# Kernel optimization log

Measured on AMD Instinct MI355X. Metric: run time of the kernel, lower is better.

## Reference

```python
import jax, jax.numpy as jnp
import numpy as np

B, S, E, H = 4, 2048, 1024, 16
D = E // H  # d_k = 64
NEG = -1000000000.0  # matches torch masked_fill constant


def setup_inputs() -> dict:
    rk = jax.random.key(0)
    kq, kk, kv, km = jax.random.split(rk, 4)
    query = jax.random.normal(kq, (B, S, E), dtype=jnp.float32)
    key = jax.random.normal(kk, (B, S, E), dtype=jnp.float32)
    value = jax.random.normal(kv, (B, S, E), dtype=jnp.float32)
    mask = jax.random.randint(km, (B, S, S), 0, 2, dtype=jnp.int32)
    return {"query": query, "key": key, "value": value, "mask": mask}


def _split_heads(x):
    # (B, S, E) -> (B, H, S, D)
    return x.reshape(B, S, H, D).transpose(0, 2, 1, 3)


def reference(query, key, value, mask):
    q = _split_heads(query)
    k = _split_heads(key)
    v = _split_heads(value)
    scale = np.float32(1.0 / np.sqrt(D))
    scores = jnp.einsum('bhqd,bhkd->bhqk', q, k) * scale  # (B,H,S,S)
    scores = jnp.where(mask[:, None, :, :] == 0, jnp.float32(NEG), scores)
    weights = jax.nn.softmax(scores, axis=-1)
    attn = jnp.einsum('bhqk,bhkd->bhqd', weights, v)  # (B,H,S,D)
    concat = attn.transpose(0, 2, 1, 3).reshape(B, S, E)
    return concat
```

## Files before the change

### kernel.cpp

```cpp
#include <hip/hip_runtime.h>
#include <hip/hip_bf16.h>
#include <math.h>

constexpr int B = 4, S = 2048, E = 1024, H = 16, D = 64;
constexpr float NEGF = -1000000000.0f;
constexpr float KSCALE = 0.125f * 1.44269504f;

typedef __attribute__((ext_vector_type(8))) short short8;
typedef __attribute__((ext_vector_type(16))) float f32x16;

__device__ inline unsigned pk2(float a, float b) {
    unsigned ua = __builtin_bit_cast(unsigned, a) + 0x8000u;
    unsigned ub = __builtin_bit_cast(unsigned, b) + 0x8000u;
    return __builtin_amdgcn_perm(ub, ua, 0x07060302u);
}
__device__ inline void gl_lds16(const void* g, void* l) {
    __builtin_amdgcn_global_load_lds(
        (const __attribute__((address_space(1))) unsigned int*)g,
        (__attribute__((address_space(3))) unsigned int*)l, 16, 0, 0);
}
__device__ inline void plswap(unsigned& a, unsigned& b) {
    asm volatile("v_permlane32_swap_b32 %0, %1" : "+v"(a), "+v"(b));
}

constexpr size_t WS_K  = 0;
constexpr size_t WS_VT = 18874368;
constexpr size_t WS_MB = 37748736;
constexpr size_t WS_NEED = 54525952;

__global__ void prep_all(const float* __restrict__ K, const float* __restrict__ V,
                         const int* __restrict__ M, char* __restrict__ ws) {
    __shared__ float Vf[64][69];
    const int bid = blockIdx.x, tid = threadIdx.x;

    {
        int g = bid * 256 + tid;
        int rowd = g >> 2, qtr = g & 3;
        int b = rowd >> 15, h = (rowd >> 11) & 15, s = rowd & 2047;
        const float* p = K + ((size_t)(b * S + s)) * E + h * 64 + qtr * 16;
        float4 v0 = *(const float4*)(p + 0),  v1 = *(const float4*)(p + 4);
        float4 v2 = *(const float4*)(p + 8),  v3 = *(const float4*)(p + 12);
        uint4 o0, o1;
        o0.x = pk2(v0.x * KSCALE, v0.y * KSCALE); o0.y = pk2(v0.z * KSCALE, v0.w * KSCALE);
        o0.z = pk2(v1.x * KSCALE, v1.y * KSCALE); o0.w = pk2(v1.z * KSCALE, v1.w * KSCALE);
        o1.x = pk2(v2.x * KSCALE, v2.y * KSCALE); o1.y = pk2(v2.z * KSCALE, v2.w * KSCALE);
        o1.z = pk2(v3.x * KSCALE, v3.y * KSCALE); o1.w = pk2(v3.z * KSCALE, v3.w * KSCALE);
        char* d = ws + WS_K + (size_t)rowd * 144 + qtr * 32;
        *(uint4*)d = o0; *(uint4*)(d + 16) = o1;
        if (qtr == 3) {
            uint4 z; z.x = z.y = z.z = z.w = 0;
            *(uint4*)(d + 32) = z;
        }
    }

    {
        int bh = bid >> 5, kt = bid & 31;
        int b = bh >> 4, h = bh & 15;
        {
            int r = tid >> 2, c4 = (tid & 3) * 16;
            const float* p = V + ((size_t)(b * S + kt * 64 + r)) * E + h * 64 + c4;
            float4 a = *(const float4*)(p + 0), bb = *(const float4*)(p + 4);
            float4 c = *(const float4*)(p + 8), dd = *(const float4*)(p + 12);
            *(float4*)&Vf[r][c4 + 0] = a;  *(float4*)&Vf[r][c4 + 4] = bb;
            *(float4*)&Vf[r][c4 + 8] = c;  *(float4*)&Vf[r][c4 + 12] = dd;
        }
        __syncthreads();
        int d = tid >> 2, sq = (tid & 3) * 16;
        float v[16];
#pragma unroll
        for (int i = 0; i < 16; ++i) v[i] = Vf[sq + i][d];
        uint4 o0, o1;
        o0.x = pk2(v[0], v[1]);   o0.y = pk2(v[2], v[3]);
        o0.z = pk2(v[4], v[5]);   o0.w = pk2(v[6], v[7]);
        o1.x = pk2(v[8], v[9]);   o1.y = pk2(v[10], v[11]);
        o1.z = pk2(v[12], v[13]); o1.w = pk2(v[14], v[15]);
        char* o = ws + WS_VT + ((size_t)(bh * 32 + kt)) * 9216 + d * 144 + sq * 2;
        *(uint4*)o = o0; *(uint4*)(o + 16) = o1;
        if (sq == 48) {
            uint4 z; z.x = z.y = z.z = z.w = 0;
            *(uint4*)(o + 32) = z;
        }
    }

    {
        unsigned* Mb = (unsigned*)(ws + WS_MB);
        const int t = bid * 256 + tid;
#pragma unroll
        for (int it = 0; it < 8; ++it) {
            int gidx = it * 524288 + t;
            int4 mv = *((const int4*)M + gidx);
            unsigned d = (mv.x ? 0xFFu : 0u) | (mv.y ? 0xFF00u : 0u)
                       | (mv.z ? 0xFF0000u : 0u) | (mv.w ? 0xFF000000u : 0u);
            int row = gidx >> 4, g = gidx & 15;
            Mb[row * 16 + (g & 1) * 8 + (g >> 1)] = d;
        }
    }
}

__global__ __launch_bounds__(512, 4)
void fa_mfma(const float* __restrict__ Q, const char* __restrict__ ws,
             float* __restrict__ O) {
    __shared__ char smem[34816];
    const int tid = threadIdx.x;
    const int w = tid >> 6, lane = tid & 63;
    const int wq = w & 3, g = w >> 2;
    const int L5 = lane & 31, h6 = lane >> 5;
    const int h = blockIdx.x & 15, b = (blockIdx.x >> 4) & 3, qt = blockIdx.x >> 6;
    const int bh = b * 16 + h;
    const int q0w = qt * 256 + wq * 64 + g * 32;

    const char* Kws  = ws + WS_K;
    const char* Vtws = ws + WS_VT;
    const int qA = q0w + L5;
    const char* mrowA = ws + WS_MB + ((size_t)(b * S + qA)) * 2048 + h6 * 32;

    short8 qf[4];
#pragma unroll
    for (int ks = 0; ks < 4; ++ks) {
        const float* qp = Q + ((size_t)(b * S + qA)) * E + h * 64 + ks * 16 + h6 * 8;
        float4 a = *(const float4*)qp;
        float4 c = *(const float4*)(qp + 4);
        uint4 u;
        u.x = pk2(a.x, a.y); u.y = pk2(a.z, a.w);
        u.z = pk2(c.x, c.y); u.w = pk2(c.z, c.w);
        qf[ks] = *(short8*)&u;
    }

    f32x16 acc[2];
#pragma unroll
    for (int mb = 0; mb < 2; ++mb) acc[mb] = (f32x16)0.0f;
    float l0 = 0.0f;

    for (int ti = 0; ti < 32; ++ti) {
        const uint4 mAl = *(const uint4*)(mrowA + ti * 64);
        const uint4 mAh = *(const uint4*)(mrowA + ti * 64 + 16);
        const unsigned mdwA[8] = {mAl.x, mAl.y, mAl.z, mAl.w, mAh.x, mAh.y, mAh.z, mAh.w};

        __syncthreads();
        {
            const char* ksrc = Kws + ((size_t)bh * S + ti * 64) * 144;
            const char* vsrc = Vtws + ((size_t)(bh * 32 + ti)) * 9216;
#pragma unroll
            for (int c = 0; c < 3; ++c) {
                int idx = c * 8 + w;
                if (idx < 18) {
                    int off = idx * 1024;
                    const char* gp = (off < 9216) ? (ksrc + off) : (vsrc + off - 9216);
                    gl_lds16(gp + lane * 16, smem + off);
                }
            }
        }
        __syncthreads();

        const char* bufK = smem;
        const char* bufV = smem + 9216;

#pragma unroll
        for (int mbK = 0; mbK < 2; ++mbK) {
            short8 kf[4];
#pragma unroll
            for (int ks = 0; ks < 4; ++ks)
                kf[ks] = *(const short8*)(bufK + (mbK * 32 + L5) * 144 + ks * 32 + h6 * 16);

            f32x16 s = (f32x16)0.0f;
            __builtin_amdgcn_s_setprio(1);
#pragma unroll
            for (int ks = 0; ks < 4; ++ks)
                s = __builtin_amdgcn_mfma_f32_32x32x16_bf16(kf[ks], qf[ks], s, 0, 0, 0);
            __builtin_amdgcn_s_setprio(0);

            float lacc = 0.0f;
            unsigned pd[8];
#pragma unroll
            for (int i = 0; i < 8; ++i) {
                float e0 = __builtin_amdgcn_exp2f(s[2 * i]);
                float e1 = __builtin_amdgcn_exp2f(s[2 * i + 1]);
                unsigned pm = pk2(e0, e1);
                const unsigned mv = mdwA[mbK * 4 + (i >> 1)];
                const unsigned am = __builtin_amdgcn_perm(
                    mv, mv, (i & 1) ? 0x03030202u : 0x01010000u);
                pm &= am;
                pd[i] = pm;
                float lo = __builtin_bit_cast(float, pm << 16);
                float hi = __builtin_bit_cast(float, pm & 0xFFFF0000u);
                lacc += lo + hi;
            }
            l0 += lacc;

            plswap(pd[0], pd[2]); plswap(pd[1], pd[3]);
            plswap(pd[4], pd[6]); plswap(pd[5], pd[7]);
            uint4 f0; f0.x = pd[0]; f0.y = pd[1]; f0.z = pd[2]; f0.w = pd[3];
            uint4 f1; f1.x = pd[4]; f1.y = pd[5]; f1.z = pd[6]; f1.w = pd[7];
            short8 pf0 = *(short8*)&f0;
            short8 pf1 = *(short8*)&f1;

#pragma unroll
            for (int mbV = 0; mbV < 2; ++mbV) {
                short8 vf0 = *(const short8*)(bufV + (mbV * 32 + L5) * 144
                                              + (mbK * 2 + 0) * 32 + h6 * 16);
                short8 vf1 = *(const short8*)(bufV + (mbV * 32 + L5) * 144
                                              + (mbK * 2 + 1) * 32 + h6 * 16);
                __builtin_amdgcn_s_setprio(1);
                acc[mbV] = __builtin_amdgcn_mfma_f32_32x32x16_bf16(vf0, pf0, acc[mbV], 0, 0, 0);
                acc[mbV] = __builtin_amdgcn_mfma_f32_32x32x16_bf16(vf1, pf1, acc[mbV], 0, 0, 0);
                __builtin_amdgcn_s_setprio(0);
            }
        }
    }

    char* const Pse = smem + wq * 8704;
    l0 += __shfl_xor(l0, 32, 64);
    const float inv0 = 1.0f / l0;
    __syncthreads();
#pragma unroll
    for (int rnd = 0; rnd < 2; ++rnd) {
        if (g == rnd) {
#pragma unroll
            for (int mb = 0; mb < 2; ++mb)
#pragma unroll
                for (int g4 = 0; g4 < 4; ++g4) {
                    float4 t;
                    t.x = acc[mb][g4 * 4 + 0] * inv0;
                    t.y = acc[mb][g4 * 4 + 1] * inv0;
                    t.z = acc[mb][g4 * 4 + 2] * inv0;
                    t.w = acc[mb][g4 * 4 + 3] * inv0;
                    *(float4*)(Pse + (L5 * 68 + mb * 32 + g4 * 8 + h6 * 4) * 4) = t;
                }
            __builtin_amdgcn_s_waitcnt(0xc07f);
            const int r16 = lane >> 4, dc = lane & 15;
#pragma unroll
            for (int i = 0; i < 8; ++i) {
                const int row = i * 4 + r16;
                float4 t = *(const float4*)(Pse + (row * 68 + dc * 4) * 4);
                *(float4*)(O + ((size_t)b * S + q0w + row) * E + h * 64 + dc * 4) = t;
            }
        }
        __syncthreads();
    }
}

constexpr int QT = 64, KT = 64, LD = D + 4;
constexpr float SCALE = 0.125f;
__global__ __launch_bounds__(256, 3)
void fa_fp32(const float* __restrict__ Q, const float* __restrict__ K,
             const float* __restrict__ V, const int* __restrict__ M,
             float* __restrict__ Out)
{
    __shared__ float Qs[QT][LD];
    __shared__ float Vs[KT][LD];
    __shared__ float KPs[KT][LD];
    const int tid = threadIdx.x, tx = tid & 15, ty = tid >> 4;
    const int bid = blockIdx.x;
    const int h = bid % H, b = (bid / H) % B, qt = bid / (H * B);
    const int q0 = qt * QT;
    {
        const int col = tx * 4;
#pragma unroll
        for (int i = 0; i < 4; ++i) {
            const int row = ty + i * 16;
            *(float4*)&Qs[row][col] = *(const float4*)&Q[((size_t)(b * S + q0 + row)) * E + h * D + col];
        }
    }
    const int qr0 = ty * 4, d0 = tx * 4;
    float acc[4][4] = {};
    float m_i[4], l_i[4];
#pragma unroll
    for (int j = 0; j < 4; ++j) { m_i[j] = -INFINITY; l_i[j] = 0.0f; }
    for (int kt = 0; kt < S; kt += KT) {
        __syncthreads();
        {
            const int col = tx * 4;
#pragma unroll
            for (int i = 0; i < 4; ++i) {
                const int row = ty + i * 16;
                const size_t g = ((size_t)(b * S + kt + row)) * E + h * D + col;
                *(float4*)&KPs[row][col] = *(const float4*)&K[g];
                *(float4*)&Vs[row][col] = *(const float4*)&V[g];
            }
        }
        __syncthreads();
        float s[4][4] = {};
#pragma unroll
        for (int d = 0; d < D; d += 4) {
            float4 a[4], bb[4];
#pragma unroll
            for (int j = 0; j < 4; ++j) a[j] = *(const float4*)&Qs[qr0 + j][d];
#pragma unroll
            for (int i = 0; i < 4; ++i) bb[i] = *(const float4*)&KPs[tx + 16 * i][d];
#pragma unroll
            for (int j = 0; j < 4; ++j)
#pragma unroll
                for (int i = 0; i < 4; ++i)
                    s[j][i] += a[j].x * bb[i].x + a[j].y * bb[i].y + a[j].z * bb[i].z + a[j].w * bb[i].w;
        }
#pragma unroll
        for (int j = 0; j < 4; ++j) {
            const int* mrow = &M[((size_t)b * S + (q0 + qr0 + j)) * S + kt];
#pragma unroll
            for (int i = 0; i < 4; ++i) {
                const int mk = mrow[tx + 16 * i];
                s[j][i] = mk ? s[j][i] * SCALE : NEGF;
            }
        }
#pragma unroll
        for (int j = 0; j < 4; ++j) {
            float tm = fmaxf(fmaxf(s[j][0], s[j][1]), fmaxf(s[j][2], s[j][3]));
#pragma unroll
            for (int off = 8; off; off >>= 1) tm = fmaxf(tm, __shfl_xor(tm, off, 16));
            const float nm = fmaxf(m_i[j], tm);
            const float alpha = __expf(m_i[j] - nm);
            m_i[j] = nm;
            float rs = 0.0f;
#pragma unroll
            for (int i = 0; i < 4; ++i) { const float p = __expf(s[j][i] - nm); s[j][i] = p; rs += p; }
#pragma unroll
            for (int off = 8; off; off >>= 1) rs += __shfl_xor(rs, off, 16);
            l_i[j] = l_i[j] * alpha + rs;
#pragma unroll
            for (int dd = 0; dd < 4; ++dd) acc[j][dd] *= alpha;
        }
        __syncthreads();
#pragma unroll
        for (int j = 0; j < 4; ++j)
#pragma unroll
            for (int i = 0; i < 4; ++i) KPs[qr0 + j][tx + 16 * i] = s[j][i];
        __syncthreads();
#pragma unroll 4
        for (int kk = 0; kk < KT; kk += 4) {
            float4 p[4], vv[4];
#pragma unroll
            for (int j = 0; j < 4; ++j) p[j] = *(const float4*)&KPs[qr0 + j][kk];
#pragma unroll
            for (int u = 0; u < 4; ++u) vv[u] = *(const float4*)&Vs[kk + u][d0];
#pragma unroll
            for (int j = 0; j < 4; ++j) {
                acc[j][0] += p[j].x * vv[0].x + p[j].y * vv[1].x + p[j].z * vv[2].x + p[j].w * vv[3].x;
                acc[j][1] += p[j].x * vv[0].y + p[j].y * vv[1].y + p[j].z * vv[2].y + p[j].w * vv[3].y;
                acc[j][2] += p[j].x * vv[0].z + p[j].y * vv[1].z + p[j].z * vv[2].z + p[j].w * vv[3].z;
                acc[j][3] += p[j].x * vv[0].w + p[j].y * vv[1].w + p[j].z * vv[2].w + p[j].w * vv[3].w;
            }
        }
    }
#pragma unroll
    for (int j = 0; j < 4; ++j) {
        const float iv = 1.0f / l_i[j];
        float4 r;
        r.x = acc[j][0] * iv; r.y = acc[j][1] * iv; r.z = acc[j][2] * iv; r.w = acc[j][3] * iv;
        *(float4*)&Out[((size_t)(b * S + q0 + qr0 + j)) * E + h * D + d0] = r;
    }
}

extern "C" void kernel_launch(void* const* d_in, const int* in_sizes, int n_in,
                              void* d_out, int out_size, void* d_ws, size_t ws_size,
                              hipStream_t stream) {
    (void)in_sizes; (void)n_in; (void)out_size;
    const float* q = (const float*)d_in[0];
    const float* k = (const float*)d_in[1];
    const float* v = (const float*)d_in[2];
    const int*   m = (const int*)d_in[3];
    float* out = (float*)d_out;

    if (ws_size >= WS_NEED) {
        char* ws = (char*)d_ws;
        prep_all<<<2048, 256, 0, stream>>>(k, v, m, ws);
        fa_mfma<<<512, 512, 0, stream>>>(q, ws, out);
    } else {
        fa_fp32<<<B * H * (S / QT), 256, 0, stream>>>(q, k, v, m, out);
    }
}
```

Before: 280.7 us.

## Process two KV tiles per barrier pair to halve synchronization count

The main loop now stages two 64-key K/V tiles into shared memory per iteration (16 iterations instead of 32), doubling the LDS staging area. This halves the number of __syncthreads barriers and load-issue phases, and loads mask words for both tiles up front. The cost is more LDS per block (36 KB), which could reduce occupancy, plus higher register pressure from the extra mask words.

```diff
diff --git a/kernel.cpp b/kernel.cpp
--- a/kernel.cpp
+++ b/kernel.cpp
@@ -100,7 +100,7 @@
 __global__ __launch_bounds__(512, 4)
 void fa_mfma(const float* __restrict__ Q, const char* __restrict__ ws,
              float* __restrict__ O) {
-    __shared__ char smem[34816];
+    __shared__ char smem[36864];
     const int tid = threadIdx.x;
     const int w = tid >> 6, lane = tid & 63;
     const int wq = w & 3, g = w >> 2;
@@ -131,79 +131,87 @@
     for (int mb = 0; mb < 2; ++mb) acc[mb] = (f32x16)0.0f;
     float l0 = 0.0f;
 
-    for (int ti = 0; ti < 32; ++ti) {
-        const uint4 mAl = *(const uint4*)(mrowA + ti * 64);
-        const uint4 mAh = *(const uint4*)(mrowA + ti * 64 + 16);
-        const unsigned mdwA[8] = {mAl.x, mAl.y, mAl.z, mAl.w, mAh.x, mAh.y, mAh.z, mAh.w};
+    for (int tp = 0; tp < 16; ++tp) {
+        const uint4 m0l = *(const uint4*)(mrowA + tp * 128);
+        const uint4 m0h = *(const uint4*)(mrowA + tp * 128 + 16);
+        const uint4 m1l = *(const uint4*)(mrowA + tp * 128 + 64);
+        const uint4 m1h = *(const uint4*)(mrowA + tp * 128 + 80);
+        const unsigned mdw0[8] = {m0l.x, m0l.y, m0l.z, m0l.w, m0h.x, m0h.y, m0h.z, m0h.w};
+        const unsigned mdw1[8] = {m1l.x, m1l.y, m1l.z, m1l.w, m1h.x, m1h.y, m1h.z, m1h.w};
 
         __syncthreads();
         {
-            const char* ksrc = Kws + ((size_t)bh * S + ti * 64) * 144;
-            const char* vsrc = Vtws + ((size_t)(bh * 32 + ti)) * 9216;
-#pragma unroll
-            for (int c = 0; c < 3; ++c) {
+            const char* ksrc = Kws + (size_t)bh * S * 144 + (size_t)tp * 18432;
+            const char* vsrc = Vtws + ((size_t)(bh * 32 + tp * 2)) * 9216;
+#pragma unroll
+            for (int c = 0; c < 5; ++c) {
                 int idx = c * 8 + w;
-                if (idx < 18) {
-                    int off = idx * 1024;
-                    const char* gp = (off < 9216) ? (ksrc + off) : (vsrc + off - 9216);
-                    gl_lds16(gp + lane * 16, smem + off);
+                if (idx < 36) {
+                    int t = (idx >= 18), j = idx - t * 18;
+                    const char* gp = (j < 9) ? (ksrc + t * 9216 + j * 1024)
+                                             : (vsrc + t * 9216 + (j - 9) * 1024);
+                    gl_lds16(gp + lane * 16, smem + t * 18432 + j * 1024);
                 }
             }
         }
         __syncthreads();
 
-        const char* bufK = smem;
-        const char* bufV = smem + 9216;
-
-#pragma unroll
-        for (int mbK = 0; mbK < 2; ++mbK) {
-            short8 kf[4];
-#pragma unroll
-            for (int ks = 0; ks < 4; ++ks)
-                kf[ks] = *(const short8*)(bufK + (mbK * 32 + L5) * 144 + ks * 32 + h6 * 16);
-
-            f32x16 s = (f32x16)0.0f;
-            __builtin_amdgcn_s_setprio(1);
-#pragma unroll
-            for (int ks = 0; ks < 4; ++ks)
-                s = __builtin_amdgcn_mfma_f32_32x32x16_bf16(kf[ks], qf[ks], s, 0, 0, 0);
-            __builtin_amdgcn_s_setprio(0);
-
-            float lacc = 0.0f;
-            unsigned pd[8];
-#pragma unroll
-            for (int i = 0; i < 8; ++i) {
-                float e0 = __builtin_amdgcn_exp2f(s[2 * i]);
-                float e1 = __builtin_amdgcn_exp2f(s[2 * i + 1]);
-                unsigned pm = pk2(e0, e1);
-                const unsigned mv = mdwA[mbK * 4 + (i >> 1)];
-                const unsigned am = __builtin_amdgcn_perm(
-                    mv, mv, (i & 1) ? 0x03030202u : 0x01010000u);
-                pm &= am;
-                pd[i] = pm;
-                float lo = __builtin_bit_cast(float, pm << 16);
-                float hi = __builtin_bit_cast(float, pm & 0xFFFF0000u);
-                lacc += lo + hi;
-            }
-            l0 += lacc;
-
-            plswap(pd[0], pd[2]); plswap(pd[1], pd[3]);
-            plswap(pd[4], pd[6]); plswap(pd[5], pd[7]);
-            uint4 f0; f0.x = pd[0]; f0.y = pd[1]; f0.z = pd[2]; f0.w = pd[3];
-            uint4 f1; f1.x = pd[4]; f1.y = pd[5]; f1.z = pd[6]; f1.w = pd[7];
-            short8 pf0 = *(short8*)&f0;
-            short8 pf1 = *(short8*)&f1;
-
-#pragma unroll
-            for (int mbV = 0; mbV < 2; ++mbV) {
-                short8 vf0 = *(const short8*)(bufV + (mbV * 32 + L5) * 144
-                                              + (mbK * 2 + 0) * 32 + h6 * 16);
-                short8 vf1 = *(const short8*)(bufV + (mbV * 32 + L5) * 144
-                                              + (mbK * 2 + 1) * 32 + h6 * 16);
+#pragma unroll
+        for (int t = 0; t < 2; ++t) {
+            const unsigned* mdwA = t ? mdw1 : mdw0;
+            const char* bufK = smem + t * 18432;
+            const char* bufV = bufK + 9216;
+
+#pragma unroll
+            for (int mbK = 0; mbK < 2; ++mbK) {
+                short8 kf[4];
+#pragma unroll
+                for (int ks = 0; ks < 4; ++ks)
+                    kf[ks] = *(const short8*)(bufK + (mbK * 32 + L5) * 144 + ks * 32 + h6 * 16);
+
+                f32x16 s = (f32x16)0.0f;
                 __builtin_amdgcn_s_setprio(1);
-                acc[mbV] = __builtin_amdgcn_mfma_f32_32x32x16_bf16(vf0, pf0, acc[mbV], 0, 0, 0);
-                acc[mbV] = __builtin_amdgcn_mfma_f32_32x32x16_bf16(vf1, pf1, acc[mbV], 0, 0, 0);
+#pragma unroll
+                for (int ks = 0; ks < 4; ++ks)
+                    s = __builtin_amdgcn_mfma_f32_32x32x16_bf16(kf[ks], qf[ks], s, 0, 0, 0);
                 __builtin_amdgcn_s_setprio(0);
+
+                float lacc = 0.0f;
+                unsigned pd[8];
+#pragma unroll
+                for (int i = 0; i < 8; ++i) {
+                    float e0 = __builtin_amdgcn_exp2f(s[2 * i]);
+                    float e1 = __builtin_amdgcn_exp2f(s[2 * i + 1]);
+                    unsigned pm = pk2(e0, e1);
+                    const unsigned mv = mdwA[mbK * 4 + (i >> 1)];
+                    const unsigned am = __builtin_amdgcn_perm(
+                        mv, mv, (i & 1) ? 0x03030202u : 0x01010000u);
+                    pm &= am;
+                    pd[i] = pm;
+                    float lo = __builtin_bit_cast(float, pm << 16);
+                    float hi = __builtin_bit_cast(float, pm & 0xFFFF0000u);
+                    lacc += lo + hi;
+                }
+                l0 += lacc;
+
+                plswap(pd[0], pd[2]); plswap(pd[1], pd[3]);
+                plswap(pd[4], pd[6]); plswap(pd[5], pd[7]);
+                uint4 f0; f0.x = pd[0]; f0.y = pd[1]; f0.z = pd[2]; f0.w = pd[3];
+                uint4 f1; f1.x = pd[4]; f1.y = pd[5]; f1.z = pd[6]; f1.w = pd[7];
+                short8 pf0 = *(short8*)&f0;
+                short8 pf1 = *(short8*)&f1;
+
+#pragma unroll
+                for (int mbV = 0; mbV < 2; ++mbV) {
+                    short8 vf0 = *(const short8*)(bufV + (mbV * 32 + L5) * 144
+                                                  + (mbK * 2 + 0) * 32 + h6 * 16);
+                    short8 vf1 = *(const short8*)(bufV + (mbV * 32 + L5) * 144
+                                                  + (mbK * 2 + 1) * 32 + h6 * 16);
+                    __builtin_amdgcn_s_setprio(1);
+                    acc[mbV] = __builtin_amdgcn_mfma_f32_32x32x16_bf16(vf0, pf0, acc[mbV], 0, 0, 0);
+                    acc[mbV] = __builtin_amdgcn_mfma_f32_32x32x16_bf16(vf1, pf1, acc[mbV], 0, 0, 0);
+                    __builtin_amdgcn_s_setprio(0);
+                }
             }
         }
     }
```

Result: no change. 285.9 us (+1.9%).
